# Kernel optimization log

Hardware: AMD Instinct MI355X
Metric: run time of the kernel (lower is better)

Reference implementation:

```python
import jax, jax.numpy as jnp
import numpy as np
from jax import lax

N_BINS = 32


def _comp_hist(dose, masks_ncv, num_voxels, n_bins):
    # dose: [N,1,D,H,W]  masks_ncv: [N,C,V]  num_voxels: [N,C]
    bw = 1.0 / n_bins
    N = dose.shape[0]
    d = dose.reshape(N, -1)  # [N,V] (C==1)
    bins = (jnp.arange(n_bins, dtype=d.dtype) * bw)  # bin edges i*bin_width

    def body(_, b):
        sig = jax.nn.sigmoid((d - b) / bw)              # [N,V]
        num = jnp.einsum('nv,ncv->c', sig, masks_ncv)   # summed over batch too (faithful to torch dim=(0,2,3,4))
        return None, num

    _, nums = lax.scan(body, None, bins)                # [B,C]
    # hist[:, i] = num / num_voxels broadcasts [C] over [N,C]
    hist = nums[None, :, :] / num_voxels[:, None, :]    # [N,B,C]
    return hist


def setup_inputs() -> dict:
    key = jax.random.key(0)
    k1, k2, k3 = jax.random.split(key, 3)
    shape = (2, 1, 128, 128, 128)
    predicted_dose = jax.random.uniform(k1, shape, jnp.float32)
    target_dose = jax.random.uniform(k2, shape, jnp.float32)
    structure_masks = jax.random.randint(k3, (2, 128, 128, 128, 10), 0, 2).astype(jnp.float32)
    return {"predicted_dose": predicted_dose, "target_dose": target_dose,
            "structure_masks": structure_masks}


def reference(predicted_dose, target_dose, structure_masks):
    N = predicted_dose.shape[0]
    # permute (0,4,1,2,3): [N,D,H,W,C] -> [N,C,D,H,W], then flatten spatial dims
    m = jnp.transpose(structure_masks, (0, 4, 1, 2, 3))
    C = m.shape[1]
    masks_ncv = m.reshape(N, C, -1)                    # [N,C,V]
    num_voxels = jnp.sum(masks_ncv, axis=2) + 1.0      # [N,C]
    ph = _comp_hist(predicted_dose, masks_ncv, num_voxels, N_BINS)
    th = _comp_hist(target_dose, masks_ncv, num_voxels, N_BINS)
    return jnp.mean((ph - th) ** 2) / N
```

## Files before the change

kernel.cpp:

```cpp
#include <hip/hip_runtime.h>

typedef __attribute__((ext_vector_type(8))) short short8;
typedef __attribute__((ext_vector_type(4))) float f32x4;
typedef __attribute__((ext_vector_type(4))) int int4v;

#define CHUNK 1024
#define NBINS 32
#define NCLS  10
#define NREP  8

__global__ __launch_bounds__(256) void dvh_main(
    const float* __restrict__ pred, const float* __restrict__ targ,
    const float* __restrict__ mask, float* __restrict__ gD, float* __restrict__ gN,
    int chunksPerN)
{
    __shared__ float2 sE[CHUNK];
    __shared__ unsigned short mT[NCLS * CHUNK];

    const int tid  = threadIdx.x;
    const int lane = tid & 63;
    const int w    = tid >> 6;
    const int n15  = lane & 15;
    const int g    = lane >> 4;

    const int chunk = blockIdx.x;
    const size_t vbase = (size_t)chunk * CHUNK;

    float4 p = ((const float4*)(pred + vbase))[tid];
    float4 t = ((const float4*)(targ + vbase))[tid];
    uint4 mv[10];
    {
        const uint4* m4g = (const uint4*)(mask + vbase * NCLS);
        #pragma unroll
        for (int k = 0; k < 10; ++k) mv[k] = m4g[k * 256 + tid];
    }

    const float K1 = __expf((float)n15);
    const float K2 = K1 * 8886110.5f;

    *(float4*)&sE[4 * tid]     = make_float4(__expf(-32.f * p.x), __expf(-32.f * t.x),
                                             __expf(-32.f * p.y), __expf(-32.f * t.y));
    *(float4*)&sE[4 * tid + 2] = make_float4(__expf(-32.f * p.z), __expf(-32.f * t.z),
                                             __expf(-32.f * p.w), __expf(-32.f * t.w));
    {
        int f0 = tid * 4;
        int vv = f0 / 10;
        int cc = f0 - vv * 10;
        #pragma unroll
        for (int k = 0; k < 10; ++k) {
            unsigned int e[4] = {mv[k].x, mv[k].y, mv[k].z, mv[k].w};
            #pragma unroll
            for (int q = 0; q < 4; ++q) {
                mT[cc * CHUNK + (((vv >> 3) ^ (cc & 7)) << 3) + (vv & 7)] =
                    (unsigned short)(e[q] >> 16);
                cc += 1;
                int wrap = (cc >= 10);
                cc -= wrap * 10;
                vv += wrap;
            }
            vv += 102;
        }
    }
    __syncthreads();

    f32x4 acc1 = {0,0,0,0};
    f32x4 acc2 = {0,0,0,0};
    f32x4 cnt  = {0,0,0,0};
    short8 ones;
    #pragma unroll
    for (int i = 0; i < 8; ++i) ones[i] = (short)0x3F80;

    const int brow = (n15 < NCLS) ? n15 : (n15 - NCLS);

    #pragma unroll
    for (int st = 0; st < 8; ++st) {
        const int vb = (w * 8 + st) * 32;
        const int v0 = vb + g * 8;
        short8 fb = *(const short8*)&mT[brow * CHUNK + (((v0 >> 3) ^ (brow & 7)) << 3)];
        const float4* e4 = (const float4*)&sE[v0];

        int u1[4], u2[4];
        #pragma unroll
        for (int j = 0; j < 4; ++j) {
            float4 q = e4[j];
            float dea = q.y - q.x, deb = q.w - q.z;
            float pa = fmaf(q.x, K1, 1.f) * fmaf(q.y, K1, 1.f);
            float pb = fmaf(q.z, K1, 1.f) * fmaf(q.w, K1, 1.f);
            float sa = dea * K1 * __builtin_amdgcn_rcpf(pa);
            float sb = deb * K1 * __builtin_amdgcn_rcpf(pb);
            unsigned h1;
            asm("v_cvt_pk_bf16_f32 %0, %1, %2" : "=v"(h1) : "v"(sa), "v"(sb));
            u1[j] = (int)h1;
            float pc = fmaf(q.x, K2, 1.f) * fmaf(q.y, K2, 1.f);
            float pd = fmaf(q.z, K2, 1.f) * fmaf(q.w, K2, 1.f);
            float sc = dea * K2 * __builtin_amdgcn_rcpf(pc);
            float sd = deb * K2 * __builtin_amdgcn_rcpf(pd);
            unsigned h2;
            asm("v_cvt_pk_bf16_f32 %0, %1, %2" : "=v"(h2) : "v"(sc), "v"(sd));
            u2[j] = (int)h2;
        }
        int4v t1 = {u1[0], u1[1], u1[2], u1[3]};
        int4v t2 = {u2[0], u2[1], u2[2], u2[3]};
        short8 A1 = __builtin_bit_cast(short8, t1);
        short8 A2 = __builtin_bit_cast(short8, t2);

        acc1 = __builtin_amdgcn_mfma_f32_16x16x32_bf16(A1, fb, acc1, 0, 0, 0);
        acc2 = __builtin_amdgcn_mfma_f32_16x16x32_bf16(A2, fb, acc2, 0, 0, 0);
        cnt  = __builtin_amdgcn_mfma_f32_16x16x32_bf16(ones, fb, cnt, 0, 0, 0);
    }
    __syncthreads();

    float* red  = (float*)mT;
    float* redN = red + 1280;

    if (n15 < NCLS) {
        #pragma unroll
        for (int r = 0; r < 4; ++r) {
            int b1 = g * 4 + r;
            red[(w * 32 + b1) * NCLS + n15]      = acc1[r];
            red[(w * 32 + 16 + b1) * NCLS + n15] = acc2[r];
        }
    }
    if (lane < NCLS) redN[w * NCLS + lane] = cnt[0];
    __syncthreads();

    const int rep = chunk & (NREP - 1);
    float* gDr = gD + rep * (NBINS * NCLS);
    float* gNr = gN + rep * (2 * NCLS);
    const int nsel = (chunk < chunksPerN) ? 0 : 1;

    for (int i = tid; i < NBINS * NCLS; i += 256) {
        float s = red[i] + red[320 + i] + red[640 + i] + red[960 + i];
        atomicAdd(&gDr[i], s);
    }
    if (tid < NCLS) {
        float s = redN[tid] + redN[10 + tid] + redN[20 + tid] + redN[30 + tid];
        atomicAdd(&gNr[nsel * NCLS + tid], s);
    }
}

__global__ __launch_bounds__(512) void dvh_final(
    const float* __restrict__ gD, const float* __restrict__ gN, float* __restrict__ out)
{
    __shared__ float red[512];
    __shared__ float nvs[2 * NCLS];
    const int t = threadIdx.x;

    if (t < 2 * NCLS) {
        float s = 1.f;
        #pragma unroll
        for (int r = 0; r < NREP; ++r) s += gN[r * (2 * NCLS) + t];
        nvs[t] = s;
    }
    float d = 0.f;
    if (t < NBINS * NCLS) {
        #pragma unroll
        for (int r = 0; r < NREP; ++r) d += gD[r * (NBINS * NCLS) + t];
    }
    __syncthreads();

    float v = 0.f;
    if (t < NBINS * NCLS) {
        int c = t % NCLS;
        float nv0 = nvs[c], nv1 = nvs[NCLS + c];
        v = d * d * (1.f / (nv0 * nv0) + 1.f / (nv1 * nv1));
    }
    red[t] = v;
    __syncthreads();
    for (int s = 256; s > 0; s >>= 1) {
        if (t < s) red[t] += red[t + s];
        __syncthreads();
    }
    if (t == 0) out[0] = red[0] * (1.f / 1280.f);
}

extern "C" void kernel_launch(void* const* d_in, const int* in_sizes, int n_in,
                              void* d_out, int out_size, void* d_ws, size_t ws_size,
                              hipStream_t stream) {
    const float* pred = (const float*)d_in[0];
    const float* targ = (const float*)d_in[1];
    const float* mask = (const float*)d_in[2];
    float* gD = (float*)d_ws;
    float* gN = (float*)((char*)d_ws + NREP * NBINS * NCLS * 4);

    hipMemsetAsync(d_ws, 0, NREP * (NBINS * NCLS + 2 * NCLS) * 4, stream);

    int totalVox    = in_sizes[0];
    int chunksTotal = totalVox / CHUNK;
    int chunksPerN  = chunksTotal / 2;

    dvh_main<<<chunksTotal, 256, 0, stream>>>(pred, targ, mask, gD, gN, chunksPerN);
    dvh_final<<<1, 512, 0, stream>>>(gD, gN, (float*)d_out);
}
```

Before: 50.08 us.

## Process two chunks per block, prefetching the second during the first's compute

Each block now handles chunk b and chunk b+nblocks (one from each batch item), so the grid is halved. The global loads for the second chunk are issued after the first chunk's shared-memory staging, so their latency overlaps the first chunk's MFMA work. Histogram partials accumulate across both chunks, which halves the reduction and atomic traffic per voxel. The cost is higher register pressure from holding the second chunk's mask data, which may lower occupancy.

```diff
diff --git a/kernel.cpp b/kernel.cpp
--- a/kernel.cpp
+++ b/kernel.cpp
@@ -12,7 +12,7 @@
 __global__ __launch_bounds__(256) void dvh_main(
     const float* __restrict__ pred, const float* __restrict__ targ,
     const float* __restrict__ mask, float* __restrict__ gD, float* __restrict__ gN,
-    int chunksPerN)
+    int nblocks)
 {
     __shared__ float2 sE[CHUNK];
     __shared__ unsigned short mT[NCLS * CHUNK];
@@ -23,32 +23,34 @@
     const int n15  = lane & 15;
     const int g    = lane >> 4;
 
-    const int chunk = blockIdx.x;
-    const size_t vbase = (size_t)chunk * CHUNK;
-
-    float4 p = ((const float4*)(pred + vbase))[tid];
-    float4 t = ((const float4*)(targ + vbase))[tid];
-    uint4 mv[10];
-    {
-        const uint4* m4g = (const uint4*)(mask + vbase * NCLS);
-        #pragma unroll
-        for (int k = 0; k < 10; ++k) mv[k] = m4g[k * 256 + tid];
-    }
+    const size_t vbaseA = (size_t)blockIdx.x * CHUNK;
+    const size_t vbaseB = (size_t)(blockIdx.x + nblocks) * CHUNK;
 
     const float K1 = __expf((float)n15);
     const float K2 = K1 * 8886110.5f;
 
-    *(float4*)&sE[4 * tid]     = make_float4(__expf(-32.f * p.x), __expf(-32.f * t.x),
-                                             __expf(-32.f * p.y), __expf(-32.f * t.y));
-    *(float4*)&sE[4 * tid + 2] = make_float4(__expf(-32.f * p.z), __expf(-32.f * t.z),
-                                             __expf(-32.f * p.w), __expf(-32.f * t.w));
-    {
-        int f0 = tid * 4;
-        int vv = f0 / 10;
-        int cc = f0 - vv * 10;
+    const int f0  = tid * 4;
+    const int vv0 = f0 / 10;
+    const int cc0 = f0 - vv0 * 10;
+
+    float4 pA = ((const float4*)(pred + vbaseA))[tid];
+    float4 tA = ((const float4*)(targ + vbaseA))[tid];
+    uint4 mvA[10];
+    {
+        const uint4* m4g = (const uint4*)(mask + vbaseA * NCLS);
+        #pragma unroll
+        for (int k = 0; k < 10; ++k) mvA[k] = m4g[k * 256 + tid];
+    }
+
+    *(float4*)&sE[4 * tid]     = make_float4(__expf(-32.f * pA.x), __expf(-32.f * tA.x),
+                                             __expf(-32.f * pA.y), __expf(-32.f * tA.y));
+    *(float4*)&sE[4 * tid + 2] = make_float4(__expf(-32.f * pA.z), __expf(-32.f * tA.z),
+                                             __expf(-32.f * pA.w), __expf(-32.f * tA.w));
+    {
+        int vv = vv0, cc = cc0;
         #pragma unroll
         for (int k = 0; k < 10; ++k) {
-            unsigned int e[4] = {mv[k].x, mv[k].y, mv[k].z, mv[k].w};
+            unsigned int e[4] = {mvA[k].x, mvA[k].y, mvA[k].z, mvA[k].w};
             #pragma unroll
             for (int q = 0; q < 4; ++q) {
                 mT[cc * CHUNK + (((vv >> 3) ^ (cc & 7)) << 3) + (vv & 7)] =
@@ -63,9 +65,19 @@
     }
     __syncthreads();
 
+    float4 pB = ((const float4*)(pred + vbaseB))[tid];
+    float4 tB = ((const float4*)(targ + vbaseB))[tid];
+    uint4 mvB[10];
+    {
+        const uint4* m4g = (const uint4*)(mask + vbaseB * NCLS);
+        #pragma unroll
+        for (int k = 0; k < 10; ++k) mvB[k] = m4g[k * 256 + tid];
+    }
+
     f32x4 acc1 = {0,0,0,0};
     f32x4 acc2 = {0,0,0,0};
-    f32x4 cnt  = {0,0,0,0};
+    f32x4 cntA = {0,0,0,0};
+    f32x4 cntB = {0,0,0,0};
     short8 ones;
     #pragma unroll
     for (int i = 0; i < 8; ++i) ones[i] = (short)0x3F80;
@@ -78,7 +90,6 @@
         const int v0 = vb + g * 8;
         short8 fb = *(const short8*)&mT[brow * CHUNK + (((v0 >> 3) ^ (brow & 7)) << 3)];
         const float4* e4 = (const float4*)&sE[v0];
-
         int u1[4], u2[4];
         #pragma unroll
         for (int j = 0; j < 4; ++j) {
@@ -103,15 +114,74 @@
         int4v t2 = {u2[0], u2[1], u2[2], u2[3]};
         short8 A1 = __builtin_bit_cast(short8, t1);
         short8 A2 = __builtin_bit_cast(short8, t2);
-
         acc1 = __builtin_amdgcn_mfma_f32_16x16x32_bf16(A1, fb, acc1, 0, 0, 0);
         acc2 = __builtin_amdgcn_mfma_f32_16x16x32_bf16(A2, fb, acc2, 0, 0, 0);
-        cnt  = __builtin_amdgcn_mfma_f32_16x16x32_bf16(ones, fb, cnt, 0, 0, 0);
-    }
-    __syncthreads();
-
-    float* red  = (float*)mT;
-    float* redN = red + 1280;
+        cntA = __builtin_amdgcn_mfma_f32_16x16x32_bf16(ones, fb, cntA, 0, 0, 0);
+    }
+    __syncthreads();
+
+    *(float4*)&sE[4 * tid]     = make_float4(__expf(-32.f * pB.x), __expf(-32.f * tB.x),
+                                             __expf(-32.f * pB.y), __expf(-32.f * tB.y));
+    *(float4*)&sE[4 * tid + 2] = make_float4(__expf(-32.f * pB.z), __expf(-32.f * tB.z),
+                                             __expf(-32.f * pB.w), __expf(-32.f * tB.w));
+    {
+        int vv = vv0, cc = cc0;
+        #pragma unroll
+        for (int k = 0; k < 10; ++k) {
+            unsigned int e[4] = {mvB[k].x, mvB[k].y, mvB[k].z, mvB[k].w};
+            #pragma unroll
+            for (int q = 0; q < 4; ++q) {
+                mT[cc * CHUNK + (((vv >> 3) ^ (cc & 7)) << 3) + (vv & 7)] =
+                    (unsigned short)(e[q] >> 16);
+                cc += 1;
+                int wrap = (cc >= 10);
+                cc -= wrap * 10;
+                vv += wrap;
+            }
+            vv += 102;
+        }
+    }
+    __syncthreads();
+
+    #pragma unroll
+    for (int st = 0; st < 8; ++st) {
+        const int vb = (w * 8 + st) * 32;
+        const int v0 = vb + g * 8;
+        short8 fb = *(const short8*)&mT[brow * CHUNK + (((v0 >> 3) ^ (brow & 7)) << 3)];
+        const float4* e4 = (const float4*)&sE[v0];
+        int u1[4], u2[4];
+        #pragma unroll
+        for (int j = 0; j < 4; ++j) {
+            float4 q = e4[j];
+            float dea = q.y - q.x, deb = q.w - q.z;
+            float pa = fmaf(q.x, K1, 1.f) * fmaf(q.y, K1, 1.f);
+            float pb = fmaf(q.z, K1, 1.f) * fmaf(q.w, K1, 1.f);
+            float sa = dea * K1 * __builtin_amdgcn_rcpf(pa);
+            float sb = deb * K1 * __builtin_amdgcn_rcpf(pb);
+            unsigned h1;
+            asm("v_cvt_pk_bf16_f32 %0, %1, %2" : "=v"(h1) : "v"(sa), "v"(sb));
+            u1[j] = (int)h1;
+            float pc = fmaf(q.x, K2, 1.f) * fmaf(q.y, K2, 1.f);
+            float pd = fmaf(q.z, K2, 1.f) * fmaf(q.w, K2, 1.f);
+            float sc = dea * K2 * __builtin_amdgcn_rcpf(pc);
+            float sd = deb * K2 * __builtin_amdgcn_rcpf(pd);
+            unsigned h2;
+            asm("v_cvt_pk_bf16_f32 %0, %1, %2" : "=v"(h2) : "v"(sc), "v"(sd));
+            u2[j] = (int)h2;
+        }
+        int4v t1 = {u1[0], u1[1], u1[2], u1[3]};
+        int4v t2 = {u2[0], u2[1], u2[2], u2[3]};
+        short8 A1 = __builtin_bit_cast(short8, t1);
+        short8 A2 = __builtin_bit_cast(short8, t2);
+        acc1 = __builtin_amdgcn_mfma_f32_16x16x32_bf16(A1, fb, acc1, 0, 0, 0);
+        acc2 = __builtin_amdgcn_mfma_f32_16x16x32_bf16(A2, fb, acc2, 0, 0, 0);
+        cntB = __builtin_amdgcn_mfma_f32_16x16x32_bf16(ones, fb, cntB, 0, 0, 0);
+    }
+    __syncthreads();
+
+    float* red   = (float*)mT;
+    float* redNA = red + 1280;
+    float* redNB = red + 1320;
 
     if (n15 < NCLS) {
         #pragma unroll
@@ -121,21 +191,25 @@
             red[(w * 32 + 16 + b1) * NCLS + n15] = acc2[r];
         }
     }
-    if (lane < NCLS) redN[w * NCLS + lane] = cnt[0];
-    __syncthreads();
-
-    const int rep = chunk & (NREP - 1);
+    if (lane < NCLS) {
+        redNA[w * NCLS + lane] = cntA[0];
+        redNB[w * NCLS + lane] = cntB[0];
+    }
+    __syncthreads();
+
+    const int rep = blockIdx.x & (NREP - 1);
     float* gDr = gD + rep * (NBINS * NCLS);
     float* gNr = gN + rep * (2 * NCLS);
-    const int nsel = (chunk < chunksPerN) ? 0 : 1;
 
     for (int i = tid; i < NBINS * NCLS; i += 256) {
         float s = red[i] + red[320 + i] + red[640 + i] + red[960 + i];
         atomicAdd(&gDr[i], s);
     }
-    if (tid < NCLS) {
-        float s = redN[tid] + redN[10 + tid] + redN[20 + tid] + redN[30 + tid];
-        atomicAdd(&gNr[nsel * NCLS + tid], s);
+    if (tid < 2 * NCLS) {
+        float* rn = (tid < NCLS) ? redNA : redNB;
+        int c = (tid < NCLS) ? tid : (tid - NCLS);
+        float s = rn[c] + rn[10 + c] + rn[20 + c] + rn[30 + c];
+        atomicAdd(&gNr[tid], s);
     }
 }
 
@@ -185,10 +259,9 @@
 
     hipMemsetAsync(d_ws, 0, NREP * (NBINS * NCLS + 2 * NCLS) * 4, stream);
 
-    int totalVox    = in_sizes[0];
-    int chunksTotal = totalVox / CHUNK;
-    int chunksPerN  = chunksTotal / 2;
-
-    dvh_main<<<chunksTotal, 256, 0, stream>>>(pred, targ, mask, gD, gN, chunksPerN);
+    int totalVox = in_sizes[0];
+    int nblocks  = totalVox / CHUNK / 2;
+
+    dvh_main<<<nblocks, 256, 0, stream>>>(pred, targ, mask, gD, gN, nblocks);
     dvh_final<<<1, 512, 0, stream>>>(gD, gN, (float*)d_out);
 }
```

Measured after the change: 51.27 us. +2.4%, slower.
